# Kernel optimization log

Hardware: AMD Instinct MI355X
Metric: run time of the kernel (lower is better)

## Reference

```python
import jax, jax.numpy as jnp
import numpy as np

EMBED = 1024
NUM_HEADS = 8
HEAD_DIM = EMBED // NUM_HEADS // 2  # 64
LAMBDA_INIT = 0.8
EPS = 1e-5


def setup_inputs() -> dict:
    key = jax.random.key(0)
    ks = jax.random.split(key, 12)
    B, T = 2, 2048
    mk = lambda k, shape, s=1.0: (jax.random.normal(k, shape, dtype=jnp.float32) * s)
    return {
        "q": mk(ks[0], (B, T, EMBED)),
        "k": mk(ks[1], (B, T, EMBED)),
        "v": mk(ks[2], (B, T, EMBED)),
        "Wq": mk(ks[3], (EMBED, EMBED), EMBED ** -0.5),
        "Wk": mk(ks[4], (EMBED, EMBED), EMBED ** -0.5),
        "Wv": mk(ks[5], (EMBED, EMBED), EMBED ** -0.5),
        "Wo": mk(ks[6], (EMBED, EMBED), EMBED ** -0.5),
        "lambda_q1": mk(ks[7], (HEAD_DIM,), 0.1),
        "lambda_k1": mk(ks[8], (HEAD_DIM,), 0.1),
        "lambda_q2": mk(ks[9], (HEAD_DIM,), 0.1),
        "lambda_k2": mk(ks[10], (HEAD_DIM,), 0.1),
    }


def reference(q, k, v, Wq, Wk, Wv, Wo, lambda_q1, lambda_k1, lambda_q2, lambda_k2):
    B, T, E = q.shape
    H, d = NUM_HEADS, HEAD_DIM
    scaling = d ** -0.5
    # projections (torch Linear: x @ W^T)
    qh = (q @ Wq.T).reshape(B, T, 2 * H, d).transpose(0, 2, 1, 3) * scaling  # [B,2H,T,d]
    kh = (k @ Wk.T).reshape(B, T, 2 * H, d).transpose(0, 2, 1, 3)            # [B,2H,T,d]
    vh = (v @ Wv.T).reshape(B, T, H, 2 * d).transpose(0, 2, 1, 3)            # [B,H,T,2d]
    # dual softmax attention over doubled heads
    attn_weights = jnp.einsum("bhtd,bhsd->bhts", qh, kh)  # [B,2H,T,S]
    attn_weights = jax.nn.softmax(attn_weights, axis=-1)
    # lambda-weighted difference
    lambda_1 = jnp.exp(jnp.sum(lambda_q1 * lambda_k1))
    lambda_2 = jnp.exp(jnp.sum(lambda_q2 * lambda_k2))
    lambda_full = lambda_1 - lambda_2 + LAMBDA_INIT
    aw = attn_weights.reshape(B, H, 2, T, T)
    aw = aw[:, :, 0] - lambda_full * aw[:, :, 1]  # [B,H,T,S]
    attn = jnp.einsum("bhts,bhsd->bhtd", aw, vh)  # [B,H,T,2d]
    # RMSNorm over last dim (no affine), then rescale
    attn = attn * jax.lax.rsqrt(jnp.mean(attn * attn, axis=-1, keepdims=True) + EPS)
    attn = attn * (1.0 - LAMBDA_INIT)
    attn = attn.transpose(0, 2, 1, 3).reshape(B, T, H * 2 * d)
    return attn @ Wo.T
```

## Files before the change

### kernel.cpp

```cpp
#include <hip/hip_runtime.h>
#include <hip/hip_bf16.h>

typedef __bf16 bf16;
typedef __attribute__((ext_vector_type(8))) __bf16 bf16x8;
typedef __attribute__((ext_vector_type(4))) __bf16 bf16x4;
typedef __attribute__((ext_vector_type(4))) float f32x4;

#define EMBED 1024
#define BB 2
#define TT 2048
#define NH 8
#define MROWS (BB * TT)

__device__ __forceinline__ void async_cp16(const void* g, void* s) {
    __builtin_amdgcn_global_load_lds((const __attribute__((address_space(1))) void*)g,
                                     (__attribute__((address_space(3))) void*)s, 16, 0, 0);
}

struct Cvt7 { const float* s[7]; bf16* d[7]; int n[7]; };

__global__ __launch_bounds__(256) void cvt_kernel(Cvt7 a) {
    const int sl = blockIdx.y;
    const float* __restrict__ s = a.s[sl];
    bf16* __restrict__ d = a.d[sl];
    int i = (blockIdx.x * 256 + threadIdx.x) * 8;
    if (i >= a.n[sl]) return;
    f32x4 x = *(const f32x4*)(s + i);
    f32x4 y = *(const f32x4*)(s + i + 4);
    bf16x8 o;
    o[0] = (bf16)x[0]; o[1] = (bf16)x[1]; o[2] = (bf16)x[2]; o[3] = (bf16)x[3];
    o[4] = (bf16)y[0]; o[5] = (bf16)y[1]; o[6] = (bf16)y[2]; o[7] = (bf16)y[3];
    *(bf16x8*)(d + i) = o;
}

struct ProjArgs { const bf16* A[3]; const bf16* Bw[3]; bf16* C[3]; float scale[3]; };

__global__ __launch_bounds__(256) void gemm_proj(ProjArgs g) {
    const int z = blockIdx.z;
    const bf16* __restrict__ A  = g.A[z];
    const bf16* __restrict__ Bw = g.Bw[z];
    bf16* __restrict__ C = g.C[z];
    const float scale = g.scale[z];

    __shared__ __align__(16) bf16 sA[128 * 32];
    __shared__ __align__(16) bf16 sB[128 * 32];
    const int tid = threadIdx.x;
    const int wave = tid >> 6, lane = tid & 63;
    const int wRow = (wave >> 1) * 64, wCol = (wave & 1) * 64;
    const int bm = blockIdx.x, bn = blockIdx.y;
    const int fr = lane & 15, fq = lane >> 4;

    f32x4 acc[4][4] = {};

    const int r = tid >> 2, jd = tid & 3;
    const int js = jd ^ ((r >> 1) & 3);
    const bf16* Ab = A + (size_t)(bm * 128 + r) * 1024 + js * 8;
    const bf16* Bb = Bw + (size_t)(bn * 128 + r) * 1024 + js * 8;

    for (int k0 = 0; k0 < 1024; k0 += 32) {
        async_cp16(Ab + k0, &sA[r * 32 + jd * 8]);
        async_cp16(Ab + (size_t)64 * 1024 + k0, &sA[(r + 64) * 32 + jd * 8]);
        async_cp16(Bb + k0, &sB[r * 32 + jd * 8]);
        async_cp16(Bb + (size_t)64 * 1024 + k0, &sB[(r + 64) * 32 + jd * 8]);
        __syncthreads();
        const int sw = (fr >> 1) & 3;
        bf16x8 af[4], bfr[4];
#pragma unroll
        for (int i = 0; i < 4; i++) {
            af[i]  = *(const bf16x8*)&sA[(wRow + 16 * i + fr) * 32 + ((fq ^ sw) * 8)];
            bfr[i] = *(const bf16x8*)&sB[(wCol + 16 * i + fr) * 32 + ((fq ^ sw) * 8)];
        }
#pragma unroll
        for (int mi = 0; mi < 4; mi++)
#pragma unroll
            for (int ni = 0; ni < 4; ni++)
                acc[mi][ni] = __builtin_amdgcn_mfma_f32_16x16x32_bf16(af[mi], bfr[ni], acc[mi][ni], 0, 0, 0);
        __syncthreads();
    }

    if (z == 2) {
#pragma unroll
        for (int mi = 0; mi < 4; mi++)
#pragma unroll
            for (int ni = 0; ni < 4; ni++) {
                int row0 = bm * 128 + wRow + 16 * mi + fq * 4;
                int col = bn * 128 + wCol + 16 * ni + fr;
                int b_ = row0 >> 11, t = row0 & 2047;
                bf16x4 w;
#pragma unroll
                for (int rr = 0; rr < 4; rr++) w[rr] = (bf16)acc[mi][ni][rr];
                *(bf16x4*)&C[((size_t)((b_ * 8 + (col >> 7)) * 128 + (col & 127))) * 2048 + t] = w;
            }
    } else {
#pragma unroll
        for (int mi = 0; mi < 4; mi++)
#pragma unroll
            for (int ni = 0; ni < 4; ni++)
#pragma unroll
                for (int rr = 0; rr < 4; rr++) {
                    int row = bm * 128 + wRow + 16 * mi + fq * 4 + rr;
                    int col = bn * 128 + wCol + 16 * ni + fr;
                    C[(size_t)row * 1024 + col] = (bf16)(acc[mi][ni][rr] * scale);
                }
    }
}

__global__ __launch_bounds__(256) void gemm_o(const bf16* __restrict__ A,
                                              const bf16* __restrict__ Bw,
                                              float* __restrict__ C) {
    __shared__ __align__(16) bf16 sA[128 * 32];
    __shared__ __align__(16) bf16 sB[64 * 32];
    const int tid = threadIdx.x;
    const int wave = tid >> 6, lane = tid & 63;
    const int wRow = (wave >> 1) * 64, wCol = (wave & 1) * 32;
    const int bm = blockIdx.x, bn = blockIdx.y;
    const int fr = lane & 15, fq = lane >> 4;

    f32x4 acc[4][2] = {};

    const int r = tid >> 2, jd = tid & 3;
    const int js = jd ^ ((r >> 1) & 3);
    const bf16* Ab = A + (size_t)(bm * 128 + r) * 1024 + js * 8;
    const bf16* Bb = Bw + (size_t)(bn * 64 + r) * 1024 + js * 8;

    for (int k0 = 0; k0 < 1024; k0 += 32) {
        async_cp16(Ab + k0, &sA[r * 32 + jd * 8]);
        async_cp16(Ab + (size_t)64 * 1024 + k0, &sA[(r + 64) * 32 + jd * 8]);
        async_cp16(Bb + k0, &sB[r * 32 + jd * 8]);
        __syncthreads();
        const int sw = (fr >> 1) & 3;
        bf16x8 af[4], bfr[2];
#pragma unroll
        for (int i = 0; i < 4; i++)
            af[i] = *(const bf16x8*)&sA[(wRow + 16 * i + fr) * 32 + ((fq ^ sw) * 8)];
#pragma unroll
        for (int i = 0; i < 2; i++)
            bfr[i] = *(const bf16x8*)&sB[(wCol + 16 * i + fr) * 32 + ((fq ^ sw) * 8)];
#pragma unroll
        for (int mi = 0; mi < 4; mi++)
#pragma unroll
            for (int ni = 0; ni < 2; ni++)
                acc[mi][ni] = __builtin_amdgcn_mfma_f32_16x16x32_bf16(af[mi], bfr[ni], acc[mi][ni], 0, 0, 0);
        __syncthreads();
    }

#pragma unroll
    for (int mi = 0; mi < 4; mi++)
#pragma unroll
        for (int ni = 0; ni < 2; ni++)
#pragma unroll
            for (int rr = 0; rr < 4; rr++) {
                int row = bm * 128 + wRow + 16 * mi + fq * 4 + rr;
                int col = bn * 64 + wCol + 16 * ni + fr;
                C[(size_t)row * 1024 + col] = acc[mi][ni][rr];
            }
}

__global__ __launch_bounds__(256, 2) void diff_attn_mfma(const bf16* __restrict__ Qp,
                                                         const bf16* __restrict__ Kp,
                                                         const bf16* __restrict__ Vt,
                                                         const float* __restrict__ lq1,
                                                         const float* __restrict__ lk1,
                                                         const float* __restrict__ lq2,
                                                         const float* __restrict__ lk2,
                                                         bf16* __restrict__ Out) {
    __shared__ __align__(16) char smem[40960];
    bf16* sK = (bf16*)smem;
    bf16* sV = (bf16*)(smem + 16384);
    bf16* sPT = (bf16*)(smem + 32768);

    const int tid = threadIdx.x;
    const int wave = tid >> 6, lane = tid & 63;
    const int ll = lane & 15, quad = lane >> 4;
    const int rt = wave & 1, hd = wave >> 1;
    const int bh = blockIdx.y, b = bh >> 3, h = bh & 7;
    const int qt = blockIdx.x;

    float lam;
    {
        float a = lq1[lane] * lk1[lane];
        float c = lq2[lane] * lk2[lane];
#pragma unroll
        for (int off = 1; off < 64; off <<= 1) { a += __shfl_xor(a, off); c += __shfl_xor(c, off); }
        lam = __expf(a) - __expf(c) + 0.8f;
    }

    bf16x8 qf[2][2];
#pragma unroll
    for (int nt = 0; nt < 2; nt++)
#pragma unroll
        for (int kc = 0; kc < 2; kc++)
            qf[nt][kc] = *(const bf16x8*)(Qp + (size_t)(b * TT + qt * 64 + rt * 32 + nt * 16 + ll) * 1024
                                          + h * 128 + hd * 64 + kc * 32 + quad * 8);

    f32x4 o[8][2] = {};
    float lp[2] = {};

    const bf16* Kbase = Kp + (size_t)(b * TT) * 1024 + h * 128;
    const bf16* Vbase = Vt + (size_t)bh * 128 * TT;
    bf16* sPw = sPT + wave * 1024;

    {
#pragma unroll
        for (int i = 0; i < 2; i++) {
            int flat = i * 256 + tid;
            int key = flat >> 4, u = flat & 15, us = u ^ (key & 15);
            async_cp16(Kbase + (size_t)key * 1024 + us * 8, &sK[key * 128 + u * 8]);
        }
#pragma unroll
        for (int i = 0; i < 2; i++) {
            int flat = i * 256 + tid;
            int dim = flat >> 2, u = flat & 3, us = u ^ (dim & 3);
            async_cp16(Vbase + (size_t)dim * TT + us * 8, &sV[dim * 32 + u * 8]);
        }
    }
    __syncthreads();

    for (int kt = 0; kt < TT / 32; kt++) {
        if (kt + 1 < TT / 32) {
            bf16* dK = sK + ((kt + 1) & 1) * 4096;
            bf16* dV = sV + ((kt + 1) & 1) * 4096;
#pragma unroll
            for (int i = 0; i < 2; i++) {
                int flat = i * 256 + tid;
                int key = flat >> 4, u = flat & 15, us = u ^ (key & 15);
                async_cp16(Kbase + (size_t)((kt + 1) * 32 + key) * 1024 + us * 8, &dK[key * 128 + u * 8]);
            }
#pragma unroll
            for (int i = 0; i < 2; i++) {
                int flat = i * 256 + tid;
                int dim = flat >> 2, u = flat & 3, us = u ^ (dim & 3);
                async_cp16(Vbase + (size_t)dim * TT + (kt + 1) * 32 + us * 8, &dV[dim * 32 + u * 8]);
            }
        }
        const bf16* cK = sK + (kt & 1) * 4096;
        const bf16* cV = sV + (kt & 1) * 4096;

        f32x4 s[2][2] = {};
#pragma unroll
        for (int mk = 0; mk < 2; mk++)
#pragma unroll
            for (int kc = 0; kc < 2; kc++) {
                int u = hd * 8 + kc * 4 + quad;
                bf16x8 kf = *(const bf16x8*)&cK[(mk * 16 + ll) * 128 + ((u ^ ll) * 8)];
#pragma unroll
                for (int nt = 0; nt < 2; nt++)
                    s[mk][nt] = __builtin_amdgcn_mfma_f32_16x16x32_bf16(kf, qf[nt][kc], s[mk][nt], 0, 0, 0);
            }

#pragma unroll
        for (int mk = 0; mk < 2; mk++)
#pragma unroll
            for (int nt = 0; nt < 2; nt++) {
                bf16x4 pb;
#pragma unroll
                for (int r = 0; r < 4; r++) {
                    float p = __expf(s[mk][nt][r]);
                    lp[nt] += p;
                    pb[r] = (bf16)p;
                }
                int u = (mk * 2 + (quad >> 1)) ^ (ll & 3);
                *(bf16x4*)&sPw[(nt * 16 + ll) * 32 + u * 8 + (quad & 1) * 4] = pb;
            }

        {
            bf16x8 pfr[2];
#pragma unroll
            for (int nt = 0; nt < 2; nt++)
                pfr[nt] = *(const bf16x8*)&sPw[(nt * 16 + ll) * 32 + ((quad ^ (ll & 3)) * 8)];
#pragma unroll
            for (int md = 0; md < 8; md++) {
                bf16x8 vf = *(const bf16x8*)&cV[(md * 16 + ll) * 32 + ((quad ^ (ll & 3)) * 8)];
#pragma unroll
                for (int nt = 0; nt < 2; nt++)
                    o[md][nt] = __builtin_amdgcn_mfma_f32_16x16x32_bf16(vf, pfr[nt], o[md][nt], 0, 0, 0);
            }
        }
        __syncthreads();
    }

    float linv[2];
#pragma unroll
    for (int nt = 0; nt < 2; nt++) {
        float ls = lp[nt];
        ls += __shfl_xor(ls, 16); ls += __shfl_xor(ls, 32);
        linv[nt] = 1.0f / ls;
    }

    __syncthreads();
    float* sE = (float*)smem;
    if (hd == 0) {
#pragma unroll
        for (int md = 0; md < 8; md++)
#pragma unroll
            for (int nt = 0; nt < 2; nt++) {
                int row = rt * 32 + nt * 16 + ll;
                int u = quad + ((md ^ (ll & 7)) << 2);
                f32x4 w;
#pragma unroll
                for (int r = 0; r < 4; r++) w[r] = o[md][nt][r] * linv[nt];
                *(f32x4*)&sE[row * 128 + u * 4] = w;
            }
    }
    __syncthreads();
    if (hd == 1) {
#pragma unroll
        for (int nt = 0; nt < 2; nt++) {
            int row = rt * 32 + nt * 16 + ll;
            float of[8][4];
            float ss = 0.f;
#pragma unroll
            for (int md = 0; md < 8; md++) {
                int u = quad + ((md ^ (ll & 7)) << 2);
                f32x4 w = *(const f32x4*)&sE[row * 128 + u * 4];
#pragma unroll
                for (int r = 0; r < 4; r++) {
                    float x = w[r] - lam * o[md][nt][r] * linv[nt];
                    of[md][r] = x;
                    ss += x * x;
                }
            }
            ss += __shfl_xor(ss, 16); ss += __shfl_xor(ss, 32);
            float rs = rsqrtf(ss * (1.0f / 128.0f) + 1e-5f) * 0.2f;
            bf16* op = Out + (size_t)(b * TT + qt * 64 + row) * 1024 + h * 128;
#pragma unroll
            for (int md = 0; md < 8; md++) {
                bf16x4 wb;
#pragma unroll
                for (int r = 0; r < 4; r++) wb[r] = (bf16)(of[md][r] * rs);
                *(bf16x4*)&op[md * 16 + quad * 4] = wb;
            }
        }
    }
}

extern "C" void kernel_launch(void* const* d_in, const int* in_sizes, int n_in,
                              void* d_out, int out_size, void* d_ws, size_t ws_size,
                              hipStream_t stream) {
    const float* q   = (const float*)d_in[0];
    const float* k   = (const float*)d_in[1];
    const float* v   = (const float*)d_in[2];
    const float* Wq  = (const float*)d_in[3];
    const float* Wk  = (const float*)d_in[4];
    const float* Wv  = (const float*)d_in[5];
    const float* Wo  = (const float*)d_in[6];
    const float* lq1 = (const float*)d_in[7];
    const float* lk1 = (const float*)d_in[8];
    const float* lq2 = (const float*)d_in[9];
    const float* lk2 = (const float*)d_in[10];

    const size_t NACT = (size_t)MROWS * EMBED;
    const size_t NW   = (size_t)EMBED * EMBED;

    char* ws = (char*)d_ws;
    bf16* qb  = (bf16*)ws; ws += NACT * 2;
    bf16* kb  = (bf16*)ws; ws += NACT * 2;
    bf16* vb  = (bf16*)ws; ws += NACT * 2;
    bf16* Wqb = (bf16*)ws; ws += NW * 2;
    bf16* Wkb = (bf16*)ws; ws += NW * 2;
    bf16* Wvb = (bf16*)ws; ws += NW * 2;
    bf16* Wob = (bf16*)ws; ws += NW * 2;
    bf16* Qp  = (bf16*)ws; ws += NACT * 2;
    bf16* Kp  = (bf16*)ws; ws += NACT * 2;
    bf16* Vtp = (bf16*)ws; ws += NACT * 2;
    bf16* Ao  = (bf16*)ws; ws += NACT * 2;

    Cvt7 cv;
    cv.s[0] = q;  cv.s[1] = k;  cv.s[2] = v;
    cv.s[3] = Wq; cv.s[4] = Wk; cv.s[5] = Wv; cv.s[6] = Wo;
    cv.d[0] = qb;  cv.d[1] = kb;  cv.d[2] = vb;
    cv.d[3] = Wqb; cv.d[4] = Wkb; cv.d[5] = Wvb; cv.d[6] = Wob;
    cv.n[0] = cv.n[1] = cv.n[2] = (int)NACT;
    cv.n[3] = cv.n[4] = cv.n[5] = cv.n[6] = (int)NW;
    cvt_kernel<<<dim3((unsigned)(NACT / 2048), 7), 256, 0, stream>>>(cv);

    ProjArgs pa;
    pa.A[0] = qb;  pa.A[1] = kb;  pa.A[2] = vb;
    pa.Bw[0] = Wqb; pa.Bw[1] = Wkb; pa.Bw[2] = Wvb;
    pa.C[0] = Qp;  pa.C[1] = Kp;  pa.C[2] = Vtp;
    pa.scale[0] = 0.125f; pa.scale[1] = 1.0f; pa.scale[2] = 1.0f;
    gemm_proj<<<dim3(MROWS / 128, EMBED / 128, 3), 256, 0, stream>>>(pa);

    diff_attn_mfma<<<dim3(TT / 64, BB * NH), 256, 0, stream>>>(Qp, Kp, Vtp, lq1, lk1, lq2, lk2, Ao);

    gemm_o<<<dim3(MROWS / 128, EMBED / 64), 256, 0, stream>>>(Ao, Wob, (float*)d_out);

    (void)in_sizes; (void)n_in; (void)out_size; (void)ws_size;
}
```

Measured before the change: 245.5 us.

## Restructure differential attention to 32x32 MFMA with 128-query blocks and split-K waves

Rewrites the attention kernel to use 512-thread blocks covering 128 queries, 64-key tiles and 32x32x16 MFMAs. The two key halves are split across waves and reduced through LDS at the end. The P operand is now built in registers via lane shuffles instead of a round trip through shared memory. The V projection is computed as a transposed GEMM (Wv times v) so it writes V^T with plain stores, which removes the scattered transpose epilogue. In exchange it uses more LDS (64KB) and larger register tiles, which may limit occupancy, and it adds more reduction steps in the epilogue.

```diff
diff --git a/kernel.cpp b/kernel.cpp
--- a/kernel.cpp
+++ b/kernel.cpp
@@ -5,6 +5,7 @@
 typedef __attribute__((ext_vector_type(8))) __bf16 bf16x8;
 typedef __attribute__((ext_vector_type(4))) __bf16 bf16x4;
 typedef __attribute__((ext_vector_type(4))) float f32x4;
+typedef __attribute__((ext_vector_type(16))) float f32x16;
 
 #define EMBED 1024
 #define BB 2
@@ -41,13 +42,15 @@
     const bf16* __restrict__ Bw = g.Bw[z];
     bf16* __restrict__ C = g.C[z];
     const float scale = g.scale[z];
+    const int bm = (z == 2) ? blockIdx.y : blockIdx.x;
+    const int bn = (z == 2) ? blockIdx.x : blockIdx.y;
+    const int ldc = (z == 2) ? 4096 : 1024;
 
     __shared__ __align__(16) bf16 sA[128 * 32];
     __shared__ __align__(16) bf16 sB[128 * 32];
     const int tid = threadIdx.x;
     const int wave = tid >> 6, lane = tid & 63;
     const int wRow = (wave >> 1) * 64, wCol = (wave & 1) * 64;
-    const int bm = blockIdx.x, bn = blockIdx.y;
     const int fr = lane & 15, fq = lane >> 4;
 
     f32x4 acc[4][4] = {};
@@ -78,31 +81,16 @@
         __syncthreads();
     }
 
-    if (z == 2) {
-#pragma unroll
-        for (int mi = 0; mi < 4; mi++)
-#pragma unroll
-            for (int ni = 0; ni < 4; ni++) {
-                int row0 = bm * 128 + wRow + 16 * mi + fq * 4;
+#pragma unroll
+    for (int mi = 0; mi < 4; mi++)
+#pragma unroll
+        for (int ni = 0; ni < 4; ni++)
+#pragma unroll
+            for (int rr = 0; rr < 4; rr++) {
+                int row = bm * 128 + wRow + 16 * mi + fq * 4 + rr;
                 int col = bn * 128 + wCol + 16 * ni + fr;
-                int b_ = row0 >> 11, t = row0 & 2047;
-                bf16x4 w;
-#pragma unroll
-                for (int rr = 0; rr < 4; rr++) w[rr] = (bf16)acc[mi][ni][rr];
-                *(bf16x4*)&C[((size_t)((b_ * 8 + (col >> 7)) * 128 + (col & 127))) * 2048 + t] = w;
-            }
-    } else {
-#pragma unroll
-        for (int mi = 0; mi < 4; mi++)
-#pragma unroll
-            for (int ni = 0; ni < 4; ni++)
-#pragma unroll
-                for (int rr = 0; rr < 4; rr++) {
-                    int row = bm * 128 + wRow + 16 * mi + fq * 4 + rr;
-                    int col = bn * 128 + wCol + 16 * ni + fr;
-                    C[(size_t)row * 1024 + col] = (bf16)(acc[mi][ni][rr] * scale);
-                }
-    }
+                C[(size_t)row * ldc + col] = (bf16)(acc[mi][ni][rr] * scale);
+            }
 }
 
 __global__ __launch_bounds__(256) void gemm_o(const bf16* __restrict__ A,
@@ -156,7 +144,7 @@
             }
 }
 
-__global__ __launch_bounds__(256, 2) void diff_attn_mfma(const bf16* __restrict__ Qp,
+__global__ __launch_bounds__(512, 2) void diff_attn_mfma(const bf16* __restrict__ Qp,
                                                          const bf16* __restrict__ Kp,
                                                          const bf16* __restrict__ Vt,
                                                          const float* __restrict__ lq1,
@@ -164,15 +152,15 @@
                                                          const float* __restrict__ lq2,
                                                          const float* __restrict__ lk2,
                                                          bf16* __restrict__ Out) {
-    __shared__ __align__(16) char smem[40960];
+    __shared__ __align__(16) char smem[65536];
     bf16* sK = (bf16*)smem;
-    bf16* sV = (bf16*)(smem + 16384);
-    bf16* sPT = (bf16*)(smem + 32768);
+    bf16* sV = (bf16*)(smem + 32768);
 
     const int tid = threadIdx.x;
-    const int wave = tid >> 6, lane = tid & 63;
-    const int ll = lane & 15, quad = lane >> 4;
-    const int rt = wave & 1, hd = wave >> 1;
+    const int lane = tid & 63;
+    const int wave = tid >> 6;
+    const int l5 = lane & 31, q2 = lane >> 5;
+    const int hd = wave & 1, qh = (wave >> 1) & 1, ks = wave >> 2;
     const int bh = blockIdx.y, b = bh >> 3, h = bh & 7;
     const int qt = blockIdx.x;
 
@@ -185,151 +173,211 @@
         lam = __expf(a) - __expf(c) + 0.8f;
     }
 
-    bf16x8 qf[2][2];
-#pragma unroll
-    for (int nt = 0; nt < 2; nt++)
-#pragma unroll
-        for (int kc = 0; kc < 2; kc++)
-            qf[nt][kc] = *(const bf16x8*)(Qp + (size_t)(b * TT + qt * 64 + rt * 32 + nt * 16 + ll) * 1024
-                                          + h * 128 + hd * 64 + kc * 32 + quad * 8);
-
-    f32x4 o[8][2] = {};
-    float lp[2] = {};
+    bf16x8 qf[2][4];
+#pragma unroll
+    for (int qrt = 0; qrt < 2; qrt++)
+#pragma unroll
+        for (int c = 0; c < 4; c++)
+            qf[qrt][c] = *(const bf16x8*)(Qp + (size_t)(b * TT + qt * 128 + qh * 64 + qrt * 32 + l5) * 1024
+                                          + h * 128 + hd * 64 + c * 16 + q2 * 8);
+
+    f32x16 o[4][2] = {};
+    float lp[2] = {0.f, 0.f};
 
     const bf16* Kbase = Kp + (size_t)(b * TT) * 1024 + h * 128;
-    const bf16* Vbase = Vt + (size_t)bh * 128 * TT;
-    bf16* sPw = sPT + wave * 1024;
-
+    const bf16* Vbase = Vt + (size_t)(h * 128) * 4096 + b * TT;
+
+#define STAGE_K(KT, BUF)                                                                   \
+    {                                                                                      \
+        bf16* dst = sK + (BUF) * 8192;                                                     \
+        _Pragma("unroll") for (int i = 0; i < 2; i++) {                                    \
+            int flat = i * 512 + tid;                                                      \
+            int key = flat >> 4, ud = flat & 15, us = ud ^ (key & 15);                     \
+            async_cp16(Kbase + (size_t)((KT) * 64 + key) * 1024 + us * 8, dst + flat * 8); \
+        }                                                                                  \
+    }
+#define STAGE_V(KT, BUF)                                                                 \
+    {                                                                                    \
+        bf16* dst = sV + (BUF) * 8192;                                                   \
+        _Pragma("unroll") for (int i = 0; i < 2; i++) {                                  \
+            int flat = i * 512 + tid;                                                    \
+            int dim = flat >> 3, ud = flat & 7, us = ud ^ (dim & 7);                     \
+            async_cp16(Vbase + (size_t)dim * 4096 + (KT) * 64 + us * 8, dst + flat * 8); \
+        }                                                                                \
+    }
+
+    STAGE_K(0, 0)
+    STAGE_V(0, 0)
+    __syncthreads();
+
+    for (int kt = 0; kt < TT / 64; kt++) {
+        if (kt + 1 < TT / 64) {
+            STAGE_K(kt + 1, (kt + 1) & 1)
+            STAGE_V(kt + 1, (kt + 1) & 1)
+        }
+        const bf16* cK = sK + (kt & 1) * 8192;
+        const bf16* cV = sV + (kt & 1) * 8192;
+
+        f32x16 s[2] = {};
+        {
+            const int key = ks * 32 + l5;
+#pragma unroll
+            for (int c = 0; c < 4; c++) {
+                int u = (hd * 8 + c * 2 + q2) ^ (key & 15);
+                bf16x8 kf = *(const bf16x8*)&cK[key * 128 + u * 8];
+                s[0] = __builtin_amdgcn_mfma_f32_32x32x16_bf16(kf, qf[0][c], s[0], 0, 0, 0);
+                s[1] = __builtin_amdgcn_mfma_f32_32x32x16_bf16(kf, qf[1][c], s[1], 0, 0, 0);
+            }
+        }
+
+        bf16x8 pf[2][2];
+#pragma unroll
+        for (int qrt = 0; qrt < 2; qrt++) {
+#pragma unroll
+            for (int r = 0; r < 16; r++) {
+                float p = __expf(s[qrt][r]);
+                s[qrt][r] = p;
+                lp[qrt] += p;
+            }
+#pragma unroll
+            for (int c2 = 0; c2 < 2; c2++) {
+                int pkk[2][2], xkk[2][2];
+#pragma unroll
+                for (int gg = 0; gg < 2; gg++) {
+                    int g = 2 * c2 + gg;
+                    bf16x4 t;
+#pragma unroll
+                    for (int rr = 0; rr < 4; rr++) t[rr] = (bf16)s[qrt][g * 4 + rr];
+                    int2 u = *(int2*)&t;
+                    pkk[gg][0] = u.x; pkk[gg][1] = u.y;
+                    xkk[gg][0] = __shfl_xor(pkk[gg][0], 32);
+                    xkk[gg][1] = __shfl_xor(pkk[gg][1], 32);
+                }
+                int4 ev;
+                ev.x = q2 ? xkk[1][0] : pkk[0][0];
+                ev.y = q2 ? xkk[1][1] : pkk[0][1];
+                ev.z = q2 ? pkk[1][0] : xkk[0][0];
+                ev.w = q2 ? pkk[1][1] : xkk[0][1];
+                pf[qrt][c2] = *(bf16x8*)&ev;
+            }
+        }
+
+#pragma unroll
+        for (int dt = 0; dt < 4; dt++) {
+            const int dim = dt * 32 + l5;
+#pragma unroll
+            for (int c2 = 0; c2 < 2; c2++) {
+                int u = (ks * 4 + c2 * 2 + q2) ^ (dim & 7);
+                bf16x8 vf = *(const bf16x8*)&cV[dim * 64 + u * 8];
+                o[dt][0] = __builtin_amdgcn_mfma_f32_32x32x16_bf16(vf, pf[0][c2], o[dt][0], 0, 0, 0);
+                o[dt][1] = __builtin_amdgcn_mfma_f32_32x32x16_bf16(vf, pf[1][c2], o[dt][1], 0, 0, 0);
+            }
+        }
+        __syncthreads();
+    }
+
+    float* sL = (float*)(smem + 54272);
     {
-#pragma unroll
-        for (int i = 0; i < 2; i++) {
-            int flat = i * 256 + tid;
-            int key = flat >> 4, u = flat & 15, us = u ^ (key & 15);
-            async_cp16(Kbase + (size_t)key * 1024 + us * 8, &sK[key * 128 + u * 8]);
-        }
-#pragma unroll
-        for (int i = 0; i < 2; i++) {
-            int flat = i * 256 + tid;
-            int dim = flat >> 2, u = flat & 3, us = u ^ (dim & 3);
-            async_cp16(Vbase + (size_t)dim * TT + us * 8, &sV[dim * 32 + u * 8]);
-        }
-    }
-    __syncthreads();
-
-    for (int kt = 0; kt < TT / 32; kt++) {
-        if (kt + 1 < TT / 32) {
-            bf16* dK = sK + ((kt + 1) & 1) * 4096;
-            bf16* dV = sV + ((kt + 1) & 1) * 4096;
-#pragma unroll
-            for (int i = 0; i < 2; i++) {
-                int flat = i * 256 + tid;
-                int key = flat >> 4, u = flat & 15, us = u ^ (key & 15);
-                async_cp16(Kbase + (size_t)((kt + 1) * 32 + key) * 1024 + us * 8, &dK[key * 128 + u * 8]);
-            }
-#pragma unroll
-            for (int i = 0; i < 2; i++) {
-                int flat = i * 256 + tid;
-                int dim = flat >> 2, u = flat & 3, us = u ^ (dim & 3);
-                async_cp16(Vbase + (size_t)dim * TT + (kt + 1) * 32 + us * 8, &dV[dim * 32 + u * 8]);
-            }
-        }
-        const bf16* cK = sK + (kt & 1) * 4096;
-        const bf16* cV = sV + (kt & 1) * 4096;
-
-        f32x4 s[2][2] = {};
-#pragma unroll
-        for (int mk = 0; mk < 2; mk++)
-#pragma unroll
-            for (int kc = 0; kc < 2; kc++) {
-                int u = hd * 8 + kc * 4 + quad;
-                bf16x8 kf = *(const bf16x8*)&cK[(mk * 16 + ll) * 128 + ((u ^ ll) * 8)];
-#pragma unroll
-                for (int nt = 0; nt < 2; nt++)
-                    s[mk][nt] = __builtin_amdgcn_mfma_f32_16x16x32_bf16(kf, qf[nt][kc], s[mk][nt], 0, 0, 0);
-            }
-
-#pragma unroll
-        for (int mk = 0; mk < 2; mk++)
-#pragma unroll
-            for (int nt = 0; nt < 2; nt++) {
-                bf16x4 pb;
-#pragma unroll
-                for (int r = 0; r < 4; r++) {
-                    float p = __expf(s[mk][nt][r]);
-                    lp[nt] += p;
-                    pb[r] = (bf16)p;
-                }
-                int u = (mk * 2 + (quad >> 1)) ^ (ll & 3);
-                *(bf16x4*)&sPw[(nt * 16 + ll) * 32 + u * 8 + (quad & 1) * 4] = pb;
-            }
-
-        {
-            bf16x8 pfr[2];
-#pragma unroll
-            for (int nt = 0; nt < 2; nt++)
-                pfr[nt] = *(const bf16x8*)&sPw[(nt * 16 + ll) * 32 + ((quad ^ (ll & 3)) * 8)];
-#pragma unroll
-            for (int md = 0; md < 8; md++) {
-                bf16x8 vf = *(const bf16x8*)&cV[(md * 16 + ll) * 32 + ((quad ^ (ll & 3)) * 8)];
-#pragma unroll
-                for (int nt = 0; nt < 2; nt++)
-                    o[md][nt] = __builtin_amdgcn_mfma_f32_16x16x32_bf16(vf, pfr[nt], o[md][nt], 0, 0, 0);
-            }
-        }
-        __syncthreads();
-    }
-
-    float linv[2];
-#pragma unroll
-    for (int nt = 0; nt < 2; nt++) {
-        float ls = lp[nt];
-        ls += __shfl_xor(ls, 16); ls += __shfl_xor(ls, 32);
-        linv[nt] = 1.0f / ls;
-    }
-
-    __syncthreads();
-    float* sE = (float*)smem;
-    if (hd == 0) {
-#pragma unroll
-        for (int md = 0; md < 8; md++)
-#pragma unroll
-            for (int nt = 0; nt < 2; nt++) {
-                int row = rt * 32 + nt * 16 + ll;
-                int u = quad + ((md ^ (ll & 7)) << 2);
-                f32x4 w;
-#pragma unroll
-                for (int r = 0; r < 4; r++) w[r] = o[md][nt][r] * linv[nt];
-                *(f32x4*)&sE[row * 128 + u * 4] = w;
-            }
-    }
-    __syncthreads();
-    if (hd == 1) {
-#pragma unroll
-        for (int nt = 0; nt < 2; nt++) {
-            int row = rt * 32 + nt * 16 + ll;
-            float of[8][4];
-            float ss = 0.f;
-#pragma unroll
-            for (int md = 0; md < 8; md++) {
-                int u = quad + ((md ^ (ll & 7)) << 2);
-                f32x4 w = *(const f32x4*)&sE[row * 128 + u * 4];
-#pragma unroll
-                for (int r = 0; r < 4; r++) {
-                    float x = w[r] - lam * o[md][nt][r] * linv[nt];
-                    of[md][r] = x;
-                    ss += x * x;
-                }
-            }
-            ss += __shfl_xor(ss, 16); ss += __shfl_xor(ss, 32);
+        float ls0 = lp[0] + __shfl_xor(lp[0], 32);
+        float ls1 = lp[1] + __shfl_xor(lp[1], 32);
+        if (ks == 0 && q2 == 0) {
+            sL[hd * 128 + qh * 64 + l5] = ls0;
+            sL[hd * 128 + qh * 64 + 32 + l5] = ls1;
+        }
+        __syncthreads();
+        if (ks == 1 && q2 == 0) {
+            sL[hd * 128 + qh * 64 + l5] += ls0;
+            sL[hd * 128 + qh * 64 + 32 + l5] += ls1;
+        }
+        __syncthreads();
+    }
+
+    float* sX = (float*)smem;
+    for (int dt = 0; dt < 4; dt++) {
+        if (ks == 1) {
+#pragma unroll
+            for (int qrt = 0; qrt < 2; qrt++) {
+                float* t = sX + ((hd * 2 + qh) * 2 + qrt) * 1056;
+#pragma unroll
+                for (int r = 0; r < 16; r++) {
+                    int row = (r & 3) + 8 * (r >> 2) + 4 * q2;
+                    t[row * 33 + l5] = o[dt][qrt][r];
+                }
+            }
+        }
+        __syncthreads();
+        if (ks == 0) {
+#pragma unroll
+            for (int qrt = 0; qrt < 2; qrt++) {
+                const float* t = sX + ((hd * 2 + qh) * 2 + qrt) * 1056;
+#pragma unroll
+                for (int r = 0; r < 16; r++) {
+                    int row = (r & 3) + 8 * (r >> 2) + 4 * q2;
+                    o[dt][qrt][r] += t[row * 33 + l5];
+                }
+            }
+        }
+        __syncthreads();
+    }
+
+    float inv0[2], inv1[2];
+    if (ks == 0 && hd == 0) {
+#pragma unroll
+        for (int qrt = 0; qrt < 2; qrt++) {
+            int qr = qh * 64 + qrt * 32 + l5;
+            inv0[qrt] = 1.0f / sL[qr];
+            inv1[qrt] = lam / sL[128 + qr];
+        }
+    }
+
+    float* sY = (float*)(smem + 36864);
+    float ssacc[2] = {0.f, 0.f};
+    for (int dt = 0; dt < 4; dt++) {
+        if (ks == 0 && hd == 1) {
+#pragma unroll
+            for (int qrt = 0; qrt < 2; qrt++) {
+                float* t = sY + (qh * 2 + qrt) * 1056;
+#pragma unroll
+                for (int r = 0; r < 16; r++) {
+                    int row = (r & 3) + 8 * (r >> 2) + 4 * q2;
+                    t[row * 33 + l5] = o[dt][qrt][r];
+                }
+            }
+        }
+        __syncthreads();
+        if (ks == 0 && hd == 0) {
+#pragma unroll
+            for (int qrt = 0; qrt < 2; qrt++) {
+                const float* t = sY + (qh * 2 + qrt) * 1056;
+#pragma unroll
+                for (int r = 0; r < 16; r++) {
+                    int row = (r & 3) + 8 * (r >> 2) + 4 * q2;
+                    float x = o[dt][qrt][r] * inv0[qrt] - inv1[qrt] * t[row * 33 + l5];
+                    o[dt][qrt][r] = x;
+                    ssacc[qrt] += x * x;
+                }
+            }
+        }
+        __syncthreads();
+    }
+
+    if (ks == 0 && hd == 0) {
+#pragma unroll
+        for (int qrt = 0; qrt < 2; qrt++) {
+            float ss = ssacc[qrt] + __shfl_xor(ssacc[qrt], 32);
             float rs = rsqrtf(ss * (1.0f / 128.0f) + 1e-5f) * 0.2f;
-            bf16* op = Out + (size_t)(b * TT + qt * 64 + row) * 1024 + h * 128;
-#pragma unroll
-            for (int md = 0; md < 8; md++) {
-                bf16x4 wb;
-#pragma unroll
-                for (int r = 0; r < 4; r++) wb[r] = (bf16)(of[md][r] * rs);
-                *(bf16x4*)&op[md * 16 + quad * 4] = wb;
-            }
+            int row = b * TT + qt * 128 + qh * 64 + qrt * 32 + l5;
+            bf16* op = Out + (size_t)row * 1024 + h * 128;
+#pragma unroll
+            for (int dt = 0; dt < 4; dt++)
+#pragma unroll
+                for (int rg = 0; rg < 4; rg++) {
+                    bf16x4 w;
+#pragma unroll
+                    for (int rr = 0; rr < 4; rr++) w[rr] = (bf16)(o[dt][qrt][rg * 4 + rr] * rs);
+                    int d0 = dt * 32 + rg * 8 + q2 * 4;
+                    *(bf16x4*)&op[d0] = w;
+                }
         }
     }
 }
@@ -375,13 +423,13 @@
     cvt_kernel<<<dim3((unsigned)(NACT / 2048), 7), 256, 0, stream>>>(cv);
 
     ProjArgs pa;
-    pa.A[0] = qb;  pa.A[1] = kb;  pa.A[2] = vb;
-    pa.Bw[0] = Wqb; pa.Bw[1] = Wkb; pa.Bw[2] = Wvb;
+    pa.A[0] = qb;  pa.A[1] = kb;  pa.A[2] = Wvb;
+    pa.Bw[0] = Wqb; pa.Bw[1] = Wkb; pa.Bw[2] = vb;
     pa.C[0] = Qp;  pa.C[1] = Kp;  pa.C[2] = Vtp;
     pa.scale[0] = 0.125f; pa.scale[1] = 1.0f; pa.scale[2] = 1.0f;
     gemm_proj<<<dim3(MROWS / 128, EMBED / 128, 3), 256, 0, stream>>>(pa);
 
-    diff_attn_mfma<<<dim3(TT / 64, BB * NH), 256, 0, stream>>>(Qp, Kp, Vtp, lq1, lk1, lq2, lk2, Ao);
+    diff_attn_mfma<<<dim3(TT / 128, BB * NH), 512, 0, stream>>>(Qp, Kp, Vtp, lq1, lk1, lq2, lk2, Ao);
 
     gemm_o<<<dim3(MROWS / 128, EMBED / 64), 256, 0, stream>>>(Ao, Wob, (float*)d_out);
 
```

Result: faster. 234.2 us (-4.6%).
